# Kernel optimization log

Hardware: AMD Instinct MI355X
Metric: run time of the kernel (lower is better)

## Reference

```python
import jax, jax.numpy as jnp
import numpy as np

_CODEBOOK = np.array([
 [-1,-1,-1,-1,-1,-1,-1,-1,-1,-1],[-1,-1,-1,-1,1,1,-1,-1,-1,1],[-1,-1,-1,1,-1,-1,-1,-1,1,1],[-1,-1,-1,1,1,1,-1,-1,1,-1],
 [-1,-1,1,-1,-1,-1,-1,1,1,-1],[-1,-1,1,-1,1,1,-1,1,1,1],[-1,-1,1,1,-1,-1,-1,1,-1,1],[-1,-1,1,1,1,1,-1,1,-1,-1],
 [-1,1,-1,-1,-1,-1,1,1,-1,-1],[-1,1,-1,-1,1,1,1,1,-1,1],[-1,1,-1,1,-1,-1,1,1,1,1],[-1,1,-1,1,1,1,1,1,1,-1],
 [-1,1,1,-1,-1,-1,1,-1,1,-1],[-1,1,1,-1,1,1,1,-1,1,1],[-1,1,1,1,-1,-1,1,-1,-1,1],[-1,1,1,1,1,1,1,-1,-1,-1],
 [1,-1,-1,-1,-1,1,1,-1,-1,-1],[1,-1,-1,-1,1,-1,1,-1,-1,1],[1,-1,-1,1,-1,1,1,-1,1,1],[1,-1,-1,1,1,-1,1,-1,1,-1],
 [1,-1,1,-1,-1,1,1,1,1,-1],[1,-1,1,-1,1,-1,1,1,1,1],[1,-1,1,1,-1,1,1,1,-1,1],[1,-1,1,1,1,-1,1,1,-1,-1],
 [1,1,-1,-1,-1,1,-1,1,-1,-1],[1,1,-1,-1,1,-1,-1,1,-1,1],[1,1,-1,1,-1,1,-1,1,1,1],[1,1,-1,1,1,-1,-1,1,1,-1],
 [1,1,1,-1,-1,1,-1,-1,1,-1],[1,1,1,-1,1,-1,-1,-1,1,1],[1,1,1,1,-1,1,-1,-1,-1,1],[1,1,1,1,1,-1,-1,-1,-1,-1]],
 dtype=np.float32)

def setup_inputs() -> dict:
    key = jax.random.key(0)
    B, N, D = 64, 65536, 10
    signal = jax.random.normal(key, (B, N, D), dtype=jnp.float32)
    codebook = jnp.asarray(_CODEBOOK)  # [32, 10]
    return {"signal": signal, "codebook": codebook}

def reference(signal, codebook):
    # Euclidean distances to all 32 codewords via Gram trick: [B, N, 32]
    x2 = jnp.sum(signal * signal, axis=-1, keepdims=True)          # [B, N, 1]
    c2 = jnp.sum(codebook * codebook, axis=-1)                      # [32]
    xc = jnp.einsum('bnd,kd->bnk', signal, codebook)                # [B, N, 32]
    d2 = jnp.maximum(x2 + c2 - 2.0 * xc, 0.0)
    distances = jnp.sqrt(d2)
    soft_assignments = jax.nn.softmax(-distances, axis=2)           # [B, N, 32]
    most_like = jnp.argmax(soft_assignments, axis=2)                # [B, N]
    softdecision = codebook[most_like]                              # [B, N, 10]
    return softdecision
```

## Files before the change

kernel.cpp:

```cpp
#include <hip/hip_runtime.h>
#include <stdint.h>

#define DIM        10
#define WPTS       128
#define WFLOATS    (WPTS * DIM)
#define WVECS      (WFLOATS / 4)
#define WAVES      4
#define THREADS    (WAVES * 64)
#define GRID       2048

static constexpr float CB[32][10] = {
 {-1,-1,-1,-1,-1,-1,-1,-1,-1,-1},{-1,-1,-1,-1,1,1,-1,-1,-1,1},{-1,-1,-1,1,-1,-1,-1,-1,1,1},{-1,-1,-1,1,1,1,-1,-1,1,-1},
 {-1,-1,1,-1,-1,-1,-1,1,1,-1},{-1,-1,1,-1,1,1,-1,1,1,1},{-1,-1,1,1,-1,-1,-1,1,-1,1},{-1,-1,1,1,1,1,-1,1,-1,-1},
 {-1,1,-1,-1,-1,-1,1,1,-1,-1},{-1,1,-1,-1,1,1,1,1,-1,1},{-1,1,-1,1,-1,-1,1,1,1,1},{-1,1,-1,1,1,1,1,1,1,-1},
 {-1,1,1,-1,-1,-1,1,-1,1,-1},{-1,1,1,-1,1,1,1,-1,1,1},{-1,1,1,1,-1,-1,1,-1,-1,1},{-1,1,1,1,1,1,1,-1,-1,-1},
 {1,-1,-1,-1,-1,1,1,-1,-1,-1},{1,-1,-1,-1,1,-1,1,-1,-1,1},{1,-1,-1,1,-1,1,1,-1,1,1},{1,-1,-1,1,1,-1,1,-1,1,-1},
 {1,-1,1,-1,-1,1,1,1,1,-1},{1,-1,1,-1,1,-1,1,1,1,1},{1,-1,1,1,-1,1,1,1,-1,1},{1,-1,1,1,1,-1,1,1,-1,-1},
 {1,1,-1,-1,-1,1,-1,1,-1,-1},{1,1,-1,-1,1,-1,-1,1,-1,1},{1,1,-1,1,-1,1,-1,1,1,1},{1,1,-1,1,1,-1,-1,1,1,-1},
 {1,1,1,-1,-1,1,-1,-1,1,-1},{1,1,1,-1,1,-1,-1,-1,1,1},{1,1,1,1,-1,1,-1,-1,-1,1},{1,1,1,1,1,-1,-1,-1,-1,-1}};

struct CBMasks { uint32_t m[32]; };
static constexpr CBMasks make_masks() {
    CBMasks r{};
    for (int k = 0; k < 32; ++k) {
        uint32_t mm = 0;
        for (int j = 0; j < DIM; ++j)
            if (CB[k][j] > 0.0f) mm |= (1u << j);
        r.m[k] = mm;
    }
    return r;
}
static constexpr CBMasks CBM = make_masks();

__device__ __forceinline__ uint32_t argmax_mask(const float* __restrict__ x) {
    float    best = -1e30f;
    uint32_t bm   = 0u;
    #pragma unroll
    for (int k = 0; k < 32; ++k) {
        float s = 0.0f;
        #pragma unroll
        for (int j = 0; j < DIM; ++j)
            s = (CB[k][j] > 0.0f) ? (s + x[j]) : (s - x[j]);
        if (s > best) { best = s; bm = CBM.m[k]; }
    }
    return bm;
}

__global__ __launch_bounds__(THREADS) void softdec_kernel(
    const float* __restrict__ sig, float* __restrict__ out, int totw)
{
    __shared__ float sIn[WAVES][WFLOATS];

    const int lane = threadIdx.x & 63;
    const int wv   = threadIdx.x >> 6;
    const int nw   = GRID * WAVES;
    float* __restrict__ sW = sIn[wv];

    const float4* __restrict__ gin = (const float4*)sig;

    int w = blockIdx.x * WAVES + wv;

    float4 p0, p1, p2, p3, p4;
    {
        const float4* __restrict__ g = gin + (size_t)w * WVECS;
        p0 = g[lane];       p1 = g[lane + 64];  p2 = g[lane + 128];
        p3 = g[lane + 192]; p4 = g[lane + 256];
    }

    while (w < totw) {
        float4* __restrict__ s4 = (float4*)sW;
        s4[lane]       = p0;  s4[lane +  64] = p1;  s4[lane + 128] = p2;
        s4[lane + 192] = p3;  s4[lane + 256] = p4;

        const int wn = w + nw;
        if (wn < totw) {
            const float4* __restrict__ g = gin + (size_t)wn * WVECS;
            p0 = g[lane];       p1 = g[lane + 64];  p2 = g[lane + 128];
            p3 = g[lane + 192]; p4 = g[lane + 256];
        }

        const float4* __restrict__ sp = (const float4*)(sW + lane * 2 * DIM);
        const float4 a0 = sp[0], a1 = sp[1], a2 = sp[2], a3 = sp[3], a4 = sp[4];
        float xA[DIM], xB[DIM];
        xA[0]=a0.x; xA[1]=a0.y; xA[2]=a0.z; xA[3]=a0.w;
        xA[4]=a1.x; xA[5]=a1.y; xA[6]=a1.z; xA[7]=a1.w;
        xA[8]=a2.x; xA[9]=a2.y;
        xB[0]=a2.z; xB[1]=a2.w;
        xB[2]=a3.x; xB[3]=a3.y; xB[4]=a3.z; xB[5]=a3.w;
        xB[6]=a4.x; xB[7]=a4.y; xB[8]=a4.z; xB[9]=a4.w;

        const uint32_t pk = argmax_mask(xA) | (argmax_mask(xB) << DIM);

        float4* __restrict__ gout = (float4*)out + (size_t)w * WVECS;
        #pragma unroll
        for (int q = 0; q < 5; ++q) {
            const int v  = q * 64 + lane;
            const int gg = 4 * v;
            const int pA = gg / DIM;
            const int cc = gg - pA * DIM;
            const int pB = (pA + 1 < WPTS) ? (pA + 1) : (WPTS - 1);
            const uint32_t pkA = (uint32_t)__builtin_amdgcn_ds_bpermute(
                                     (pA >> 1) << 2, (int)pk);
            const uint32_t pkB = (uint32_t)__builtin_amdgcn_ds_bpermute(
                                     (pB >> 1) << 2, (int)pk);
            const uint32_t A = (pkA >> ((pA & 1) * DIM)) & 0x3FFu;
            const uint32_t B = (pkB >> ((pB & 1) * DIM)) & 0x3FFu;
            const uint32_t mm = (A >> cc) | (B << (DIM - cc));
            float4 o;
            o.x = __uint_as_float(0xBF800000u ^ ((mm        & 1u) << 31));
            o.y = __uint_as_float(0xBF800000u ^ (((mm >> 1) & 1u) << 31));
            o.z = __uint_as_float(0xBF800000u ^ (((mm >> 2) & 1u) << 31));
            o.w = __uint_as_float(0xBF800000u ^ (((mm >> 3) & 1u) << 31));
            gout[v] = o;
        }
        w = wn;
    }
}

extern "C" void kernel_launch(void* const* d_in, const int* in_sizes, int n_in,
                              void* d_out, int out_size, void* d_ws, size_t ws_size,
                              hipStream_t stream) {
    const float* sig = (const float*)d_in[0];
    float* out = (float*)d_out;
    const int total = in_sizes[0];
    const int pts   = total / DIM;
    const int totw  = pts / WPTS;
    softdec_kernel<<<GRID, THREADS, 0, stream>>>(sig, out, totw);
}
```

Measured before the change: 284.1 us.

## Double-buffer global prefetch two chunks ahead and use nontemporal output stores

The register prefetch is deepened from one chunk to two, using two alternating register buffers and a manually unrolled loop. This keeps more global loads in flight per wave to hide memory latency. Output stores become nontemporal so the write stream is less likely to pollute cache. Scheduling fences are added around the LDS staging. In exchange it uses more registers, which may reduce occupancy, and the fences limit how freely the compiler can reorder instructions.

```diff
diff --git a/kernel.cpp b/kernel.cpp
--- a/kernel.cpp
+++ b/kernel.cpp
@@ -8,6 +8,8 @@
 #define WAVES      4
 #define THREADS    (WAVES * 64)
 #define GRID       2048
+
+typedef float f32x4 __attribute__((ext_vector_type(4)));
 
 static constexpr float CB[32][10] = {
  {-1,-1,-1,-1,-1,-1,-1,-1,-1,-1},{-1,-1,-1,-1,1,1,-1,-1,-1,1},{-1,-1,-1,1,-1,-1,-1,-1,1,1},{-1,-1,-1,1,1,1,-1,-1,1,-1},
@@ -46,6 +48,74 @@
     return bm;
 }
 
+struct Buf { float4 v0, v1, v2, v3, v4; };
+
+__device__ __forceinline__ Buf load_chunk(const float4* __restrict__ g, int lane) {
+    Buf b;
+    b.v0 = g[lane];       b.v1 = g[lane +  64]; b.v2 = g[lane + 128];
+    b.v3 = g[lane + 192]; b.v4 = g[lane + 256];
+    return b;
+}
+
+__device__ __forceinline__ void wave_order_fence() {
+    __builtin_amdgcn_sched_barrier(0);
+    __builtin_amdgcn_wave_barrier();
+    __builtin_amdgcn_sched_barrier(0);
+    asm volatile("" ::: "memory");
+}
+
+__device__ __forceinline__ void do_chunk(
+    Buf& b, int w, int wpre, int totw, int lane,
+    float* __restrict__ sW,
+    const float4* __restrict__ gin, float* __restrict__ out)
+{
+    float4* __restrict__ s4 = (float4*)sW;
+    s4[lane]       = b.v0;  s4[lane +  64] = b.v1;  s4[lane + 128] = b.v2;
+    s4[lane + 192] = b.v3;  s4[lane + 256] = b.v4;
+
+    wave_order_fence();
+
+    if (wpre < totw) b = load_chunk(gin + (size_t)wpre * WVECS, lane);
+
+    const float4* __restrict__ sp = (const float4*)(sW + lane * 2 * DIM);
+    const float4 a0 = sp[0], a1 = sp[1], a2 = sp[2], a3 = sp[3], a4 = sp[4];
+
+    wave_order_fence();
+
+    float xA[DIM], xB[DIM];
+    xA[0]=a0.x; xA[1]=a0.y; xA[2]=a0.z; xA[3]=a0.w;
+    xA[4]=a1.x; xA[5]=a1.y; xA[6]=a1.z; xA[7]=a1.w;
+    xA[8]=a2.x; xA[9]=a2.y;
+    xB[0]=a2.z; xB[1]=a2.w;
+    xB[2]=a3.x; xB[3]=a3.y; xB[4]=a3.z; xB[5]=a3.w;
+    xB[6]=a4.x; xB[7]=a4.y; xB[8]=a4.z; xB[9]=a4.w;
+
+    const uint32_t pk = argmax_mask(xA) | (argmax_mask(xB) << DIM);
+
+    f32x4* __restrict__ gout = (f32x4*)out + (size_t)w * WVECS;
+    #pragma unroll
+    for (int q = 0; q < 5; ++q) {
+        const int v  = q * 64 + lane;
+        const int gg = 4 * v;
+        const int pA = gg / DIM;
+        const int cc = gg - pA * DIM;
+        const int pB = (pA + 1 < WPTS) ? (pA + 1) : (WPTS - 1);
+        const uint32_t pkA = (uint32_t)__builtin_amdgcn_ds_bpermute(
+                                 (pA >> 1) << 2, (int)pk);
+        const uint32_t pkB = (uint32_t)__builtin_amdgcn_ds_bpermute(
+                                 (pB >> 1) << 2, (int)pk);
+        const uint32_t A = (pkA >> ((pA & 1) * DIM)) & 0x3FFu;
+        const uint32_t B = (pkB >> ((pB & 1) * DIM)) & 0x3FFu;
+        const uint32_t mm = (A >> cc) | (B << (DIM - cc));
+        f32x4 o;
+        o.x = __uint_as_float(0xBF800000u ^ ((mm        & 1u) << 31));
+        o.y = __uint_as_float(0xBF800000u ^ (((mm >> 1) & 1u) << 31));
+        o.z = __uint_as_float(0xBF800000u ^ (((mm >> 2) & 1u) << 31));
+        o.w = __uint_as_float(0xBF800000u ^ (((mm >> 3) & 1u) << 31));
+        __builtin_nontemporal_store(o, gout + v);
+    }
+}
+
 __global__ __launch_bounds__(THREADS) void softdec_kernel(
     const float* __restrict__ sig, float* __restrict__ out, int totw)
 {
@@ -55,65 +125,20 @@
     const int wv   = threadIdx.x >> 6;
     const int nw   = GRID * WAVES;
     float* __restrict__ sW = sIn[wv];
-
     const float4* __restrict__ gin = (const float4*)sig;
 
     int w = blockIdx.x * WAVES + wv;
 
-    float4 p0, p1, p2, p3, p4;
-    {
-        const float4* __restrict__ g = gin + (size_t)w * WVECS;
-        p0 = g[lane];       p1 = g[lane + 64];  p2 = g[lane + 128];
-        p3 = g[lane + 192]; p4 = g[lane + 256];
-    }
+    Buf A = load_chunk(gin + (size_t)w * WVECS, lane);
+    Buf B;
+    if (w + nw < totw) B = load_chunk(gin + (size_t)(w + nw) * WVECS, lane);
 
     while (w < totw) {
-        float4* __restrict__ s4 = (float4*)sW;
-        s4[lane]       = p0;  s4[lane +  64] = p1;  s4[lane + 128] = p2;
-        s4[lane + 192] = p3;  s4[lane + 256] = p4;
-
-        const int wn = w + nw;
-        if (wn < totw) {
-            const float4* __restrict__ g = gin + (size_t)wn * WVECS;
-            p0 = g[lane];       p1 = g[lane + 64];  p2 = g[lane + 128];
-            p3 = g[lane + 192]; p4 = g[lane + 256];
-        }
-
-        const float4* __restrict__ sp = (const float4*)(sW + lane * 2 * DIM);
-        const float4 a0 = sp[0], a1 = sp[1], a2 = sp[2], a3 = sp[3], a4 = sp[4];
-        float xA[DIM], xB[DIM];
-        xA[0]=a0.x; xA[1]=a0.y; xA[2]=a0.z; xA[3]=a0.w;
-        xA[4]=a1.x; xA[5]=a1.y; xA[6]=a1.z; xA[7]=a1.w;
-        xA[8]=a2.x; xA[9]=a2.y;
-        xB[0]=a2.z; xB[1]=a2.w;
-        xB[2]=a3.x; xB[3]=a3.y; xB[4]=a3.z; xB[5]=a3.w;
-        xB[6]=a4.x; xB[7]=a4.y; xB[8]=a4.z; xB[9]=a4.w;
-
-        const uint32_t pk = argmax_mask(xA) | (argmax_mask(xB) << DIM);
-
-        float4* __restrict__ gout = (float4*)out + (size_t)w * WVECS;
-        #pragma unroll
-        for (int q = 0; q < 5; ++q) {
-            const int v  = q * 64 + lane;
-            const int gg = 4 * v;
-            const int pA = gg / DIM;
-            const int cc = gg - pA * DIM;
-            const int pB = (pA + 1 < WPTS) ? (pA + 1) : (WPTS - 1);
-            const uint32_t pkA = (uint32_t)__builtin_amdgcn_ds_bpermute(
-                                     (pA >> 1) << 2, (int)pk);
-            const uint32_t pkB = (uint32_t)__builtin_amdgcn_ds_bpermute(
-                                     (pB >> 1) << 2, (int)pk);
-            const uint32_t A = (pkA >> ((pA & 1) * DIM)) & 0x3FFu;
-            const uint32_t B = (pkB >> ((pB & 1) * DIM)) & 0x3FFu;
-            const uint32_t mm = (A >> cc) | (B << (DIM - cc));
-            float4 o;
-            o.x = __uint_as_float(0xBF800000u ^ ((mm        & 1u) << 31));
-            o.y = __uint_as_float(0xBF800000u ^ (((mm >> 1) & 1u) << 31));
-            o.z = __uint_as_float(0xBF800000u ^ (((mm >> 2) & 1u) << 31));
-            o.w = __uint_as_float(0xBF800000u ^ (((mm >> 3) & 1u) << 31));
-            gout[v] = o;
-        }
-        w = wn;
+        do_chunk(A, w, w + 2 * nw, totw, lane, sW, gin, out);
+        w += nw;
+        if (w >= totw) break;
+        do_chunk(B, w, w + 2 * nw, totw, lane, sW, gin, out);
+        w += nw;
     }
 }
 
```

Result: no change. 289.6 us (+1.9%).
